# Optimization experiments

Hardware: AMD Instinct MI355X
Metric: run time of the kernel (lower is better)

## Reference

```python
import jax, jax.numpy as jnp
import numpy as np

N = 256   # units (waveguides)
L = 256   # num_layers (rectangular mesh: L == N)
B = 16384 # batch
TWO_PI = 2.0 * np.pi


def _perm_indices():
    # Rectangular-mesh column permutations: alternate +/-1 circular shifts so
    # successive columns couple (0,1),(2,3),... then (1,2),(3,4),...; final
    # permutation undoes the net shift (perm_layers has L+1 entries).
    ar = np.arange(N)
    shifts = [0] + [(1 if l % 2 == 1 else -1) for l in range(1, L)]
    perms = [(ar + s) % N for s in shifts]
    perms.append((ar - sum(shifts)) % N)
    return np.asarray(perms, dtype=np.int32)  # (L+1, N)


def setup_inputs() -> dict:
    key = jax.random.key(0)
    ks = jax.random.split(key, 5)
    x_re = jax.random.normal(ks[0], (B, N), jnp.float32)
    x_im = jax.random.normal(ks[1], (B, N), jnp.float32)
    theta = jax.random.uniform(ks[2], (L, N // 2), jnp.float32) * TWO_PI
    phi = jax.random.uniform(ks[3], (L, N // 2), jnp.float32) * TWO_PI
    gamma = jax.random.uniform(ks[4], (N,), jnp.float32) * TWO_PI
    perm_idx = jnp.asarray(_perm_indices())
    pp = np.arange(N).reshape(-1, 2)[:, ::-1].reshape(-1)  # [1,0,3,2,...]
    pairwise_perm_idx = jnp.asarray(pp, dtype=jnp.int32)
    return dict(x_re=x_re, x_im=x_im, theta=theta, phi=phi, gamma=gamma,
                perm_idx=perm_idx, pairwise_perm_idx=pairwise_perm_idx)


def _mesh_diag_offdiag(theta, phi):
    # Bloch basis, differential internal arrangement: +theta/2 on top port
    # (even waveguide), -theta/2 on bottom port (odd waveguide).
    t = theta.T  # (N/2, L)
    internal = jnp.stack([t * 0.5, -t * 0.5], axis=1).reshape(N, L)
    # single-mode external arrangement: phi on top port, 0 on bottom.
    external = jnp.stack([phi.T, jnp.zeros_like(phi.T)], axis=1).reshape(N, L)
    ipsl = jnp.exp(1j * internal)   # (N, L) complex64
    epsl = jnp.exp(1j * external)
    up = lambda a: jnp.roll(a, -1, axis=0)   # roll_tensor(x, up=True)
    dn = lambda a: jnp.roll(a, 1, axis=0)    # roll_tensor(x)
    e = jnp.float32(0.5)  # ideal 50:50 splitters -> all mzi_error_tensors = 0.5
    # hadamard = False branch of Mesh.mesh_layers
    s11 = e * ipsl - e * up(ipsl)
    s22 = dn(-e * ipsl + e * up(ipsl))
    s12 = 1j * dn(e * ipsl + e * up(ipsl))
    s21 = 1j * (e * ipsl + e * up(ipsl))
    diag = epsl * (s11 + s22) * 0.5
    off = dn(epsl) * (s21 + s12) * 0.5
    return diag.T, off.T  # (L, N)


def reference(x_re, x_im, theta, phi, gamma, perm_idx, pairwise_perm_idx):
    diag, off = _mesh_diag_offdiag(theta, phi)
    # include_diagonal_phases: input phase screen exp(i*gamma)
    x = (x_re + 1j * x_im) * jnp.exp(1j * gamma)[None, :]

    def step(x, lay):
        perm, d, o = lay
        x = jnp.take(x, perm, axis=-1)                              # PermutationLayer
        x = x * d + jnp.take(x * o, pairwise_perm_idx, axis=-1)     # MZI couple
        return x, None

    x, _ = jax.lax.scan(step, x, (perm_idx[:L], diag, off))
    x = jnp.take(x, perm_idx[L], axis=-1)  # right_perm of final layer
    return jnp.stack([jnp.real(x), jnp.imag(x)])  # (2, B, N) float32
```

## Files before the change

### kernel.cpp

```cpp
#include <hip/hip_runtime.h>
#include <math.h>

#define NN 256
#define LL 256
#define BB 16384

typedef __attribute__((ext_vector_type(8))) short short8;
typedef __attribute__((ext_vector_type(4))) float f32x4;


__global__ void coef_kernel(const float* __restrict__ theta,
                            const float* __restrict__ phi,
                            const float* __restrict__ gamma,
                            float4* __restrict__ coef) {
    int idx = blockIdx.x * blockDim.x + threadIdx.x;
    if (idx >= LL * NN) return;
    int l = idx >> 8, j = idx & 255;
    int u = l & 1;
    int n = (j - u) & 255;
    int m = n ^ 1;
    const float* th = theta + l * (NN / 2);
    const float* ph = phi + l * (NN / 2);

    auto ipsl = [&](int k, double& re, double& im) {
        k &= 255;
        double a = (double)th[k >> 1] * ((k & 1) ? -0.5 : 0.5);
        double s, c; sincos(a, &s, &c); re = c; im = s;
    };
    double s, c;
    double inr, ini, ipr, ipi, imr, imi;
    ipsl(n, inr, ini); ipsl(n + 1, ipr, ipi); ipsl(n - 1, imr, imi);
    double enr = 1.0, eni = 0.0;
    if (!(n & 1)) { sincos((double)ph[n >> 1], &s, &c); enr = c; eni = s; }
    double dr = 2.0 * inr - ipr - imr;
    double di = 2.0 * ini - ipi - imi;
    double Dre = 0.25 * (enr * dr - eni * di);
    double Dim = 0.25 * (enr * di + eni * dr);
    ipsl(m, inr, ini); ipsl(m + 1, ipr, ipi); ipsl(m - 1, imr, imi);
    int mm = (m - 1) & 255;
    double emr = 1.0, emi = 0.0;
    if (!(mm & 1)) { sincos((double)ph[mm >> 1], &s, &c); emr = c; emi = s; }
    double orv = 2.0 * inr + ipr + imr;
    double oiv = 2.0 * ini + ipi + imi;
    double tre = emr * orv - emi * oiv;
    double tim = emr * oiv + emi * orv;
    double Ore = -0.25 * tim;
    double Oim =  0.25 * tre;

    if (l == 0) {
        double gs, gc;
        sincos((double)gamma[j], &gs, &gc);
        double a2 = Dre * gc - Dim * gs, b2 = Dre * gs + Dim * gc;
        Dre = a2; Dim = b2;
        sincos((double)gamma[j ^ 1], &gs, &gc);
        a2 = Ore * gc - Oim * gs; b2 = Ore * gs + Oim * gc;
        Ore = a2; Oim = b2;
    }
    coef[l * 256 + (j & 7) * 32 + (j >> 3)] =
        make_float4((float)Dre, (float)Dim, (float)Ore, (float)Oim);
}

__device__ __forceinline__ float2 mzi(float2 cD, float2 cO, float2 y, float2 p) {
    float2 t;
    asm("v_pk_mul_f32 %0, %1, %2 op_sel:[1,1] op_sel_hi:[1,0] neg_lo:[1,0]"
        : "=v"(t) : "v"(cO), "v"(p));
    asm("v_pk_fma_f32 %0, %1, %2, %0 op_sel:[0,0,0] op_sel_hi:[0,1,1]"
        : "+v"(t) : "v"(cO), "v"(p));
    asm("v_pk_fma_f32 %0, %1, %2, %0 op_sel:[1,1,0] op_sel_hi:[1,0,1] neg_lo:[1,0,0]"
        : "+v"(t) : "v"(cD), "v"(y));
    asm("v_pk_fma_f32 %0, %1, %2, %0 op_sel:[0,0,0] op_sel_hi:[0,1,1]"
        : "+v"(t) : "v"(cD), "v"(y));
    return t;
}
__device__ __forceinline__ float2 D_(float4 c) { return make_float2(c.x, c.y); }
__device__ __forceinline__ float2 O_(float4 c) { return make_float2(c.z, c.w); }

__global__ __launch_bounds__(256) void prop_kernel(const float4* __restrict__ coef,
                                                   float2* __restrict__ PA,
                                                   float2* __restrict__ PB) {
    const int lane = threadIdx.x & 63;
    const int wave = threadIdx.x >> 6;
    const int l32  = lane & 31;
    const int half = lane >> 5;
    const int gid  = blockIdx.x * 4 + wave;
    const int mhalf = gid >> 7;
    const int row  = ((gid & 127) << 1) | half;
    const int l0   = mhalf ? 128 : 0;
    const int idxL4 = (((lane & 32) | ((lane - 1) & 31))) << 2;
    const int idxR4 = (((lane & 32) | ((lane + 1) & 31))) << 2;

    float2 y[8];
#pragma unroll
    for (int j = 0; j < 8; ++j)
        y[j] = make_float2((8 * l32 + j == row) ? 1.f : 0.f, 0.f);

    const float4* cp = coef + l32;
    auto loadl = [&](int l, float4& c0, float4& c1, float4& c2, float4& c3,
                            float4& c4, float4& c5, float4& c6, float4& c7) {
        const float4* p = cp + l * 256;
        c0 = p[0 * 32]; c1 = p[1 * 32]; c2 = p[2 * 32]; c3 = p[3 * 32];
        c4 = p[4 * 32]; c5 = p[5 * 32]; c6 = p[6 * 32]; c7 = p[7 * 32];
    };

    float4 a0, a1, a2, a3, a4, a5, a6, a7;
    float4 b0, b1, b2, b3, b4, b5, b6, b7;
    loadl(l0, a0, a1, a2, a3, a4, a5, a6, a7);

#pragma unroll 1
    for (int it = 0; it < 64; ++it) {
        loadl(l0 + 2 * it + 1, b0, b1, b2, b3, b4, b5, b6, b7);
        {
            float2 t0 = y[0], t1 = y[1], t2 = y[2], t3 = y[3];
            float2 t4 = y[4], t5 = y[5], t6 = y[6], t7 = y[7];
            y[0] = mzi(D_(a0), O_(a0), t0, t1);
            y[1] = mzi(D_(a1), O_(a1), t1, t0);
            y[2] = mzi(D_(a2), O_(a2), t2, t3);
            y[3] = mzi(D_(a3), O_(a3), t3, t2);
            y[4] = mzi(D_(a4), O_(a4), t4, t5);
            y[5] = mzi(D_(a5), O_(a5), t5, t4);
            y[6] = mzi(D_(a6), O_(a6), t6, t7);
            y[7] = mzi(D_(a7), O_(a7), t7, t6);
        }
        if (it < 63) loadl(l0 + 2 * it + 2, a0, a1, a2, a3, a4, a5, a6, a7);
        {
            float2 t0 = y[0], t1 = y[1], t2 = y[2], t3 = y[3];
            float2 t4 = y[4], t5 = y[5], t6 = y[6], t7 = y[7];
            float2 plo, phi2;
            plo.x  = __int_as_float(__builtin_amdgcn_ds_bpermute(idxL4, __float_as_int(t7.x)));
            plo.y  = __int_as_float(__builtin_amdgcn_ds_bpermute(idxL4, __float_as_int(t7.y)));
            phi2.x = __int_as_float(__builtin_amdgcn_ds_bpermute(idxR4, __float_as_int(t0.x)));
            phi2.y = __int_as_float(__builtin_amdgcn_ds_bpermute(idxR4, __float_as_int(t0.y)));
            y[1] = mzi(D_(b1), O_(b1), t1, t2);
            y[2] = mzi(D_(b2), O_(b2), t2, t1);
            y[3] = mzi(D_(b3), O_(b3), t3, t4);
            y[4] = mzi(D_(b4), O_(b4), t4, t3);
            y[5] = mzi(D_(b5), O_(b5), t5, t6);
            y[6] = mzi(D_(b6), O_(b6), t6, t5);
            y[0] = mzi(D_(b0), O_(b0), t0, plo);
            y[7] = mzi(D_(b7), O_(b7), t7, phi2);
        }
    }

    float2* P = mhalf ? PB : PA;
#pragma unroll
    for (int j = 0; j < 8; ++j)
        P[row * 256 + 8 * l32 + j] = y[j];
}

__global__ __launch_bounds__(256) void combine_kernel(const float2* __restrict__ PA,
                                                      const float2* __restrict__ PB,
                                                      float2* __restrict__ Cm) {
    int i = blockIdx.x, j = threadIdx.x;
    float accr = 0.f, acci = 0.f;
#pragma unroll 4
    for (int k = 0; k < 256; ++k) {
        float2 a = PA[i * 256 + k];
        float2 b = PB[k * 256 + j];
        accr += a.x * b.x - a.y * b.y;
        acci += a.x * b.y + a.y * b.x;
    }
    Cm[i * 256 + j] = make_float2(accr, acci);
}

__device__ __forceinline__ unsigned short bf16rne(float f) {
    unsigned int u = __float_as_uint(f);
    unsigned int r = (u + 0x7FFFu + ((u >> 16) & 1u)) >> 16;
    return (unsigned short)r;
}
__device__ __forceinline__ float bf16f(unsigned short h) {
    return __uint_as_float(((unsigned int)h) << 16);
}
__device__ __forceinline__ void split3(float v, unsigned short& h0,
                                       unsigned short& h1, unsigned short& h2) {
    h0 = bf16rne(v);        float r1 = v - bf16f(h0);
    h1 = bf16rne(r1);       float r2 = r1 - bf16f(h1);
    h2 = bf16rne(r2);
}

__global__ __launch_bounds__(256) void wsplit_kernel(const float2* __restrict__ Cm,
                                                     unsigned short* __restrict__ Wt) {
    int idx = blockIdx.x * 256 + threadIdx.x;
    int n = idx >> 9, k = idx & 511;
    float w;
    if (k < 256) {
        float2 c = Cm[k * 256 + (n & 255)];
        w = (n < 256) ? c.x : c.y;
    } else {
        float2 c = Cm[(k - 256) * 256 + (n & 255)];
        w = (n < 256) ? -c.y : c.x;
    }
    unsigned short h0, h1, h2;
    split3(w, h0, h1, h2);
    Wt[0 * 262144 + n * 512 + k] = h0;
    Wt[1 * 262144 + n * 512 + k] = h1;
    Wt[2 * 262144 + n * 512 + k] = h2;
}

__global__ __launch_bounds__(256, 2) void gemm_kernel(
        const float* __restrict__ x_re, const float* __restrict__ x_im,
        const unsigned short* __restrict__ Wt, float* __restrict__ out) {
    __shared__ unsigned short XL[3][128][40];
    __shared__ unsigned short WL[3][128][40];

    const int t    = threadIdx.x;
    const int lane = t & 63;
    const int wave = t >> 6;
    const int wm   = wave >> 1, wn = wave & 1;
    const int nt = blockIdx.x & 3, mt = blockIdx.x >> 2;
    const int m0 = mt * 128, n0 = nt * 128;
    const int lr = lane & 15, lg = lane >> 4;

    f32x4 acc[4][4];
#pragma unroll
    for (int a = 0; a < 4; ++a)
#pragma unroll
        for (int b = 0; b < 4; ++b) acc[a][b] = (f32x4)0.f;

#pragma unroll 1
    for (int ks = 0; ks < 16; ++ks) {
        const int k0 = ks * 32;
        const float* xsrc = (k0 < 256) ? x_re : x_im;
        const int kcol = k0 & 255;
#pragma unroll
        for (int r = 0; r < 4; ++r) {
            int F = r * 256 + t;
            int row = F >> 3, g = F & 7;
            float4 v = ((const float4*)xsrc)[(m0 + row) * 64 + (kcol >> 2) + g];
            unsigned short h0[4], h1[4], h2[4];
            split3(v.x, h0[0], h1[0], h2[0]);
            split3(v.y, h0[1], h1[1], h2[1]);
            split3(v.z, h0[2], h1[2], h2[2]);
            split3(v.w, h0[3], h1[3], h2[3]);
            *(ushort4*)&XL[0][row][g * 4] = make_ushort4(h0[0], h0[1], h0[2], h0[3]);
            *(ushort4*)&XL[1][row][g * 4] = make_ushort4(h1[0], h1[1], h1[2], h1[3]);
            *(ushort4*)&XL[2][row][g * 4] = make_ushort4(h2[0], h2[1], h2[2], h2[3]);
        }
#pragma unroll
        for (int r = 0; r < 6; ++r) {
            int U = r * 256 + t;
            int p = U >> 9, rem = U & 511;
            int n = rem >> 2, ku = (rem & 3) * 8;
            uint4 v = ((const uint4*)Wt)[p * 32768 + (n0 + n) * 64 + ((k0 + ku) >> 3)];
            *(uint4*)&WL[p][n][ku] = v;
        }
        __syncthreads();

        short8 bfr[3][4];
#pragma unroll
        for (int p = 0; p < 3; ++p)
#pragma unroll
            for (int ni = 0; ni < 4; ++ni)
                bfr[p][ni] = *(const short8*)&WL[p][wn * 64 + ni * 16 + lr][lg * 8];

#pragma unroll
        for (int i = 0; i < 3; ++i) {
            short8 af[4];
#pragma unroll
            for (int mi = 0; mi < 4; ++mi)
                af[mi] = *(const short8*)&XL[i][wm * 64 + mi * 16 + lr][lg * 8];
#pragma unroll
            for (int j = 0; j < 3; ++j) {
                if (i + j > 2) continue;
#pragma unroll
                for (int mi = 0; mi < 4; ++mi)
#pragma unroll
                    for (int ni = 0; ni < 4; ++ni)
                        acc[mi][ni] = __builtin_amdgcn_mfma_f32_16x16x32_bf16(
                            af[mi], bfr[j][ni], acc[mi][ni], 0, 0, 0);
            }
        }
        __syncthreads();
    }

#pragma unroll
    for (int mi = 0; mi < 4; ++mi) {
#pragma unroll
        for (int ni = 0; ni < 4; ++ni) {
            int nglob = n0 + wn * 64 + ni * 16 + lr;
            float* dst = (nglob < 256)
                       ? out + (size_t)(nglob)
                       : out + (size_t)BB * 256 + (nglob - 256);
#pragma unroll
            for (int e = 0; e < 4; ++e) {
                int m = m0 + wm * 64 + mi * 16 + lg * 4 + e;
                dst[(size_t)m * 256] = acc[mi][ni][e];
            }
        }
    }
}

extern "C" void kernel_launch(void* const* d_in, const int* in_sizes, int n_in,
                              void* d_out, int out_size, void* d_ws, size_t ws_size,
                              hipStream_t stream) {
    const float* x_re  = (const float*)d_in[0];
    const float* x_im  = (const float*)d_in[1];
    const float* theta = (const float*)d_in[2];
    const float* phi   = (const float*)d_in[3];
    const float* gamma = (const float*)d_in[4];

    char* ws = (char*)d_ws;
    float4* coef        = (float4*)ws;
    float2* PA          = (float2*)(ws + (1 << 20));
    float2* PB          = (float2*)(ws + (1 << 20) + (512 << 10));
    float2* Cm          = (float2*)(ws + (2 << 20));
    unsigned short* Wt  = (unsigned short*)(ws + (2 << 20) + (512 << 10));

    hipLaunchKernelGGL(coef_kernel, dim3(256), dim3(256), 0, stream,
                       theta, phi, gamma, coef);
    hipLaunchKernelGGL(prop_kernel, dim3(64), dim3(256), 0, stream, coef, PA, PB);
    hipLaunchKernelGGL(combine_kernel, dim3(256), dim3(256), 0, stream, PA, PB, Cm);
    hipLaunchKernelGGL(wsplit_kernel, dim3(1024), dim3(256), 0, stream, Cm, Wt);
    hipLaunchKernelGGL(gemm_kernel, dim3(512), dim3(256), 0, stream,
                       x_re, x_im, Wt, (float*)d_out);
}
```

Measured before the change: 198.1 us.

## Precompute sincos tables, fuse combine with weight split, prefetch GEMM tiles

After: 238.4 us. +20.4%, slower.

```diff
diff --git a/kernel.cpp b/kernel.cpp
--- a/kernel.cpp
+++ b/kernel.cpp
@@ -9,8 +9,21 @@
 typedef __attribute__((ext_vector_type(4))) float f32x4;
 
 
-__global__ void coef_kernel(const float* __restrict__ theta,
-                            const float* __restrict__ phi,
+__global__ void tab_kernel(const float* __restrict__ theta,
+                           const float* __restrict__ phi,
+                           double2* __restrict__ ipt,
+                           double2* __restrict__ ept) {
+    int idx = blockIdx.x * blockDim.x + threadIdx.x;
+    if (idx >= LL * 128) return;
+    double s, c;
+    sincos((double)theta[idx] * 0.5, &s, &c);
+    ipt[idx] = make_double2(c, s);
+    sincos((double)phi[idx], &s, &c);
+    ept[idx] = make_double2(c, s);
+}
+
+__global__ void coef_kernel(const double2* __restrict__ ipt,
+                            const double2* __restrict__ ept,
                             const float* __restrict__ gamma,
                             float4* __restrict__ coef) {
     int idx = blockIdx.x * blockDim.x + threadIdx.x;
@@ -19,19 +32,18 @@
     int u = l & 1;
     int n = (j - u) & 255;
     int m = n ^ 1;
-    const float* th = theta + l * (NN / 2);
-    const float* ph = phi + l * (NN / 2);
+    const double2* ip = ipt + l * 128;
+    const double2* ep = ept + l * 128;
 
     auto ipsl = [&](int k, double& re, double& im) {
         k &= 255;
-        double a = (double)th[k >> 1] * ((k & 1) ? -0.5 : 0.5);
-        double s, c; sincos(a, &s, &c); re = c; im = s;
+        double2 v = ip[k >> 1];
+        re = v.x; im = (k & 1) ? -v.y : v.y;
     };
-    double s, c;
     double inr, ini, ipr, ipi, imr, imi;
     ipsl(n, inr, ini); ipsl(n + 1, ipr, ipi); ipsl(n - 1, imr, imi);
     double enr = 1.0, eni = 0.0;
-    if (!(n & 1)) { sincos((double)ph[n >> 1], &s, &c); enr = c; eni = s; }
+    if (!(n & 1)) { double2 v = ep[n >> 1]; enr = v.x; eni = v.y; }
     double dr = 2.0 * inr - ipr - imr;
     double di = 2.0 * ini - ipi - imi;
     double Dre = 0.25 * (enr * dr - eni * di);
@@ -39,7 +51,7 @@
     ipsl(m, inr, ini); ipsl(m + 1, ipr, ipi); ipsl(m - 1, imr, imi);
     int mm = (m - 1) & 255;
     double emr = 1.0, emi = 0.0;
-    if (!(mm & 1)) { sincos((double)ph[mm >> 1], &s, &c); emr = c; emi = s; }
+    if (!(mm & 1)) { double2 v = ep[mm >> 1]; emr = v.x; emi = v.y; }
     double orv = 2.0 * inr + ipr + imr;
     double oiv = 2.0 * ini + ipi + imi;
     double tre = emr * orv - emi * oiv;
@@ -48,12 +60,12 @@
     double Oim =  0.25 * tre;
 
     if (l == 0) {
-        double gs, gc;
-        sincos((double)gamma[j], &gs, &gc);
-        double a2 = Dre * gc - Dim * gs, b2 = Dre * gs + Dim * gc;
+        double s, c;
+        sincos((double)gamma[j], &s, &c);
+        double a2 = Dre * c - Dim * s, b2 = Dre * s + Dim * c;
         Dre = a2; Dim = b2;
-        sincos((double)gamma[j ^ 1], &gs, &gc);
-        a2 = Ore * gc - Oim * gs; b2 = Ore * gs + Oim * gc;
+        sincos((double)gamma[j ^ 1], &s, &c);
+        a2 = Ore * c - Oim * s; b2 = Ore * s + Oim * c;
         Ore = a2; Oim = b2;
     }
     coef[l * 256 + (j & 7) * 32 + (j >> 3)] =
@@ -83,23 +95,27 @@
     const int l32  = lane & 31;
     const int half = lane >> 5;
     const int gid  = blockIdx.x * 4 + wave;
-    const int mhalf = gid >> 7;
-    const int row  = ((gid & 127) << 1) | half;
+    const int mhalf = gid >> 6;
+    const int c4   = (gid & 63) * 4;
     const int l0   = mhalf ? 128 : 0;
     const int idxL4 = (((lane & 32) | ((lane - 1) & 31))) << 2;
     const int idxR4 = (((lane & 32) | ((lane + 1) & 31))) << 2;
 
-    float2 y[8];
-#pragma unroll
-    for (int j = 0; j < 8; ++j)
-        y[j] = make_float2((8 * l32 + j == row) ? 1.f : 0.f, 0.f);
+    float2 y[2][8];
+#pragma unroll
+    for (int s2 = 0; s2 < 2; ++s2) {
+        int row = c4 + 2 * s2 + half;
+#pragma unroll
+        for (int j = 0; j < 8; ++j)
+            y[s2][j] = make_float2((8 * l32 + j == row) ? 1.f : 0.f, 0.f);
+    }
 
     const float4* cp = coef + l32;
     auto loadl = [&](int l, float4& c0, float4& c1, float4& c2, float4& c3,
-                            float4& c4, float4& c5, float4& c6, float4& c7) {
+                            float4& c4_, float4& c5, float4& c6, float4& c7) {
         const float4* p = cp + l * 256;
         c0 = p[0 * 32]; c1 = p[1 * 32]; c2 = p[2 * 32]; c3 = p[3 * 32];
-        c4 = p[4 * 32]; c5 = p[5 * 32]; c6 = p[6 * 32]; c7 = p[7 * 32];
+        c4_ = p[4 * 32]; c5 = p[5 * 32]; c6 = p[6 * 32]; c7 = p[7 * 32];
     };
 
     float4 a0, a1, a2, a3, a4, a5, a6, a7;
@@ -109,123 +125,136 @@
 #pragma unroll 1
     for (int it = 0; it < 64; ++it) {
         loadl(l0 + 2 * it + 1, b0, b1, b2, b3, b4, b5, b6, b7);
-        {
-            float2 t0 = y[0], t1 = y[1], t2 = y[2], t3 = y[3];
-            float2 t4 = y[4], t5 = y[5], t6 = y[6], t7 = y[7];
-            y[0] = mzi(D_(a0), O_(a0), t0, t1);
-            y[1] = mzi(D_(a1), O_(a1), t1, t0);
-            y[2] = mzi(D_(a2), O_(a2), t2, t3);
-            y[3] = mzi(D_(a3), O_(a3), t3, t2);
-            y[4] = mzi(D_(a4), O_(a4), t4, t5);
-            y[5] = mzi(D_(a5), O_(a5), t5, t4);
-            y[6] = mzi(D_(a6), O_(a6), t6, t7);
-            y[7] = mzi(D_(a7), O_(a7), t7, t6);
+#pragma unroll
+        for (int s2 = 0; s2 < 2; ++s2) {
+            float2 t0 = y[s2][0], t1 = y[s2][1], t2 = y[s2][2], t3 = y[s2][3];
+            float2 t4 = y[s2][4], t5 = y[s2][5], t6 = y[s2][6], t7 = y[s2][7];
+            y[s2][0] = mzi(D_(a0), O_(a0), t0, t1);
+            y[s2][1] = mzi(D_(a1), O_(a1), t1, t0);
+            y[s2][2] = mzi(D_(a2), O_(a2), t2, t3);
+            y[s2][3] = mzi(D_(a3), O_(a3), t3, t2);
+            y[s2][4] = mzi(D_(a4), O_(a4), t4, t5);
+            y[s2][5] = mzi(D_(a5), O_(a5), t5, t4);
+            y[s2][6] = mzi(D_(a6), O_(a6), t6, t7);
+            y[s2][7] = mzi(D_(a7), O_(a7), t7, t6);
         }
         if (it < 63) loadl(l0 + 2 * it + 2, a0, a1, a2, a3, a4, a5, a6, a7);
-        {
-            float2 t0 = y[0], t1 = y[1], t2 = y[2], t3 = y[3];
-            float2 t4 = y[4], t5 = y[5], t6 = y[6], t7 = y[7];
+#pragma unroll
+        for (int s2 = 0; s2 < 2; ++s2) {
+            float2 t0 = y[s2][0], t1 = y[s2][1], t2 = y[s2][2], t3 = y[s2][3];
+            float2 t4 = y[s2][4], t5 = y[s2][5], t6 = y[s2][6], t7 = y[s2][7];
             float2 plo, phi2;
             plo.x  = __int_as_float(__builtin_amdgcn_ds_bpermute(idxL4, __float_as_int(t7.x)));
             plo.y  = __int_as_float(__builtin_amdgcn_ds_bpermute(idxL4, __float_as_int(t7.y)));
             phi2.x = __int_as_float(__builtin_amdgcn_ds_bpermute(idxR4, __float_as_int(t0.x)));
             phi2.y = __int_as_float(__builtin_amdgcn_ds_bpermute(idxR4, __float_as_int(t0.y)));
-            y[1] = mzi(D_(b1), O_(b1), t1, t2);
-            y[2] = mzi(D_(b2), O_(b2), t2, t1);
-            y[3] = mzi(D_(b3), O_(b3), t3, t4);
-            y[4] = mzi(D_(b4), O_(b4), t4, t3);
-            y[5] = mzi(D_(b5), O_(b5), t5, t6);
-            y[6] = mzi(D_(b6), O_(b6), t6, t5);
-            y[0] = mzi(D_(b0), O_(b0), t0, plo);
-            y[7] = mzi(D_(b7), O_(b7), t7, phi2);
+            y[s2][1] = mzi(D_(b1), O_(b1), t1, t2);
+            y[s2][2] = mzi(D_(b2), O_(b2), t2, t1);
+            y[s2][3] = mzi(D_(b3), O_(b3), t3, t4);
+            y[s2][4] = mzi(D_(b4), O_(b4), t4, t3);
+            y[s2][5] = mzi(D_(b5), O_(b5), t5, t6);
+            y[s2][6] = mzi(D_(b6), O_(b6), t6, t5);
+            y[s2][0] = mzi(D_(b0), O_(b0), t0, plo);
+            y[s2][7] = mzi(D_(b7), O_(b7), t7, phi2);
         }
     }
 
     float2* P = mhalf ? PB : PA;
 #pragma unroll
-    for (int j = 0; j < 8; ++j)
-        P[row * 256 + 8 * l32 + j] = y[j];
-}
-
-__global__ __launch_bounds__(256) void combine_kernel(const float2* __restrict__ PA,
-                                                      const float2* __restrict__ PB,
-                                                      float2* __restrict__ Cm) {
+    for (int s2 = 0; s2 < 2; ++s2) {
+        int row = c4 + 2 * s2 + half;
+#pragma unroll
+        for (int j = 0; j < 8; ++j)
+            P[row * 256 + 8 * l32 + j] = y[s2][j];
+    }
+}
+
+__device__ __forceinline__ unsigned short bf16rne(float f) {
+    unsigned int u2 = __float_as_uint(f);
+    unsigned int r = (u2 + 0x7FFFu + ((u2 >> 16) & 1u)) >> 16;
+    return (unsigned short)r;
+}
+__device__ __forceinline__ float bf16f(unsigned short h) {
+    return __uint_as_float(((unsigned int)h) << 16);
+}
+__device__ __forceinline__ void split3(float v, unsigned short& h0,
+                                       unsigned short& h1, unsigned short& h2) {
+    h0 = bf16rne(v);        float r1 = v - bf16f(h0);
+    h1 = bf16rne(r1);       float r2 = r1 - bf16f(h1);
+    h2 = bf16rne(r2);
+}
+
+__global__ __launch_bounds__(256) void combineW_kernel(const float2* __restrict__ PA,
+                                                       const float2* __restrict__ PB,
+                                                       unsigned short* __restrict__ Wt) {
     int i = blockIdx.x, j = threadIdx.x;
     float accr = 0.f, acci = 0.f;
-#pragma unroll 4
+#pragma unroll 8
     for (int k = 0; k < 256; ++k) {
         float2 a = PA[i * 256 + k];
         float2 b = PB[k * 256 + j];
         accr += a.x * b.x - a.y * b.y;
         acci += a.x * b.y + a.y * b.x;
     }
-    Cm[i * 256 + j] = make_float2(accr, acci);
-}
-
-__device__ __forceinline__ unsigned short bf16rne(float f) {
-    unsigned int u = __float_as_uint(f);
-    unsigned int r = (u + 0x7FFFu + ((u >> 16) & 1u)) >> 16;
-    return (unsigned short)r;
-}
-__device__ __forceinline__ float bf16f(unsigned short h) {
-    return __uint_as_float(((unsigned int)h) << 16);
-}
-__device__ __forceinline__ void split3(float v, unsigned short& h0,
-                                       unsigned short& h1, unsigned short& h2) {
-    h0 = bf16rne(v);        float r1 = v - bf16f(h0);
-    h1 = bf16rne(r1);       float r2 = r1 - bf16f(h1);
-    h2 = bf16rne(r2);
-}
-
-__global__ __launch_bounds__(256) void wsplit_kernel(const float2* __restrict__ Cm,
-                                                     unsigned short* __restrict__ Wt) {
-    int idx = blockIdx.x * 256 + threadIdx.x;
-    int n = idx >> 9, k = idx & 511;
-    float w;
-    if (k < 256) {
-        float2 c = Cm[k * 256 + (n & 255)];
-        w = (n < 256) ? c.x : c.y;
-    } else {
-        float2 c = Cm[(k - 256) * 256 + (n & 255)];
-        w = (n < 256) ? -c.y : c.x;
-    }
-    unsigned short h0, h1, h2;
-    split3(w, h0, h1, h2);
-    Wt[0 * 262144 + n * 512 + k] = h0;
-    Wt[1 * 262144 + n * 512 + k] = h1;
-    Wt[2 * 262144 + n * 512 + k] = h2;
+    unsigned short r0, r1, r2, i0, i1, i2, n0, n1, n2;
+    split3(accr, r0, r1, r2);
+    split3(acci, i0, i1, i2);
+    split3(-acci, n0, n1, n2);
+    unsigned short* W0 = Wt;
+    unsigned short* W1 = Wt + 262144;
+    unsigned short* W2 = Wt + 524288;
+    W0[j * 512 + i] = r0;           W1[j * 512 + i] = r1;           W2[j * 512 + i] = r2;
+    W0[(j + 256) * 512 + i] = i0;   W1[(j + 256) * 512 + i] = i1;   W2[(j + 256) * 512 + i] = i2;
+    W0[j * 512 + i + 256] = n0;     W1[j * 512 + i + 256] = n1;     W2[j * 512 + i + 256] = n2;
+    W0[(j + 256) * 512 + i + 256] = r0;
+    W1[(j + 256) * 512 + i + 256] = r1;
+    W2[(j + 256) * 512 + i + 256] = r2;
 }
 
 __global__ __launch_bounds__(256, 2) void gemm_kernel(
         const float* __restrict__ x_re, const float* __restrict__ x_im,
         const unsigned short* __restrict__ Wt, float* __restrict__ out) {
-    __shared__ unsigned short XL[3][128][40];
-    __shared__ unsigned short WL[3][128][40];
+    __shared__ unsigned short XL[3][128][42];
+    __shared__ unsigned short WL[3][128][42];
 
     const int t    = threadIdx.x;
     const int lane = t & 63;
     const int wave = t >> 6;
     const int wm   = wave >> 1, wn = wave & 1;
-    const int nt = blockIdx.x & 3, mt = blockIdx.x >> 2;
+    const int Lb = (blockIdx.x & 7) * 64 + (blockIdx.x >> 3);
+    const int mt = Lb >> 2, nt = Lb & 3;
     const int m0 = mt * 128, n0 = nt * 128;
     const int lr = lane & 15, lg = lane >> 4;
 
-    f32x4 acc[4][4];
-#pragma unroll
-    for (int a = 0; a < 4; ++a)
-#pragma unroll
-        for (int b = 0; b < 4; ++b) acc[a][b] = (f32x4)0.f;
-
-#pragma unroll 1
-    for (int ks = 0; ks < 16; ++ks) {
+    float4 xv[4];
+    uint4  wv[6];
+    const int F   = t;
+    const int Un  = t;
+
+    auto load_tiles = [&](int ks) {
         const int k0 = ks * 32;
         const float* xsrc = (k0 < 256) ? x_re : x_im;
         const int kcol = k0 & 255;
 #pragma unroll
         for (int r = 0; r < 4; ++r) {
-            int F = r * 256 + t;
-            int row = F >> 3, g = F & 7;
-            float4 v = ((const float4*)xsrc)[(m0 + row) * 64 + (kcol >> 2) + g];
+            int Fi = r * 256 + F;
+            int row = Fi >> 3, g = Fi & 7;
+            xv[r] = ((const float4*)xsrc)[(m0 + row) * 64 + (kcol >> 2) + g];
+        }
+#pragma unroll
+        for (int r = 0; r < 6; ++r) {
+            int U = r * 256 + Un;
+            int p = U >> 9, rem = U & 511;
+            int n = rem >> 2, ku = (rem & 3) * 8;
+            wv[r] = ((const uint4*)Wt)[p * 32768 + (n0 + n) * 64 + ((k0 + ku) >> 3)];
+        }
+    };
+    auto write_tiles = [&]() {
+#pragma unroll
+        for (int r = 0; r < 4; ++r) {
+            int Fi = r * 256 + F;
+            int row = Fi >> 3, g = Fi & 7;
+            float4 v = xv[r];
             unsigned short h0[4], h1[4], h2[4];
             split3(v.x, h0[0], h1[0], h2[0]);
             split3(v.y, h0[1], h1[1], h2[1]);
@@ -237,13 +266,26 @@
         }
 #pragma unroll
         for (int r = 0; r < 6; ++r) {
-            int U = r * 256 + t;
+            int U = r * 256 + Un;
             int p = U >> 9, rem = U & 511;
             int n = rem >> 2, ku = (rem & 3) * 8;
-            uint4 v = ((const uint4*)Wt)[p * 32768 + (n0 + n) * 64 + ((k0 + ku) >> 3)];
-            *(uint4*)&WL[p][n][ku] = v;
-        }
-        __syncthreads();
+            *(uint4*)&WL[p][n][ku] = wv[r];
+        }
+    };
+
+    f32x4 acc[4][4];
+#pragma unroll
+    for (int a = 0; a < 4; ++a)
+#pragma unroll
+        for (int b = 0; b < 4; ++b) acc[a][b] = (f32x4)0.f;
+
+    load_tiles(0);
+    write_tiles();
+    __syncthreads();
+
+#pragma unroll 1
+    for (int ks = 0; ks < 16; ++ks) {
+        if (ks < 15) load_tiles(ks + 1);
 
         short8 bfr[3][4];
 #pragma unroll
@@ -251,7 +293,6 @@
 #pragma unroll
             for (int ni = 0; ni < 4; ++ni)
                 bfr[p][ni] = *(const short8*)&WL[p][wn * 64 + ni * 16 + lr][lg * 8];
-
 #pragma unroll
         for (int i = 0; i < 3; ++i) {
             short8 af[4];
@@ -259,16 +300,18 @@
             for (int mi = 0; mi < 4; ++mi)
                 af[mi] = *(const short8*)&XL[i][wm * 64 + mi * 16 + lr][lg * 8];
 #pragma unroll
-            for (int j = 0; j < 3; ++j) {
-                if (i + j > 2) continue;
+            for (int jj = 0; jj < 3; ++jj) {
+                if (i + jj > 2) continue;
 #pragma unroll
                 for (int mi = 0; mi < 4; ++mi)
 #pragma unroll
                     for (int ni = 0; ni < 4; ++ni)
                         acc[mi][ni] = __builtin_amdgcn_mfma_f32_16x16x32_bf16(
-                            af[mi], bfr[j][ni], acc[mi][ni], 0, 0, 0);
+                            af[mi], bfr[jj][ni], acc[mi][ni], 0, 0, 0);
             }
         }
+        __syncthreads();
+        if (ks < 15) write_tiles();
         __syncthreads();
     }
 
@@ -278,7 +321,7 @@
         for (int ni = 0; ni < 4; ++ni) {
             int nglob = n0 + wn * 64 + ni * 16 + lr;
             float* dst = (nglob < 256)
-                       ? out + (size_t)(nglob)
+                       ? out + (size_t)nglob
                        : out + (size_t)BB * 256 + (nglob - 256);
 #pragma unroll
             for (int e = 0; e < 4; ++e) {
@@ -302,14 +345,16 @@
     float4* coef        = (float4*)ws;
     float2* PA          = (float2*)(ws + (1 << 20));
     float2* PB          = (float2*)(ws + (1 << 20) + (512 << 10));
-    float2* Cm          = (float2*)(ws + (2 << 20));
-    unsigned short* Wt  = (unsigned short*)(ws + (2 << 20) + (512 << 10));
-
+    unsigned short* Wt  = (unsigned short*)(ws + (2 << 20));
+    double2* ipt        = (double2*)(ws + (3 << 20) + (512 << 10));
+    double2* ept        = (double2*)(ws + (4 << 20));
+
+    hipLaunchKernelGGL(tab_kernel, dim3(128), dim3(256), 0, stream,
+                       theta, phi, ipt, ept);
     hipLaunchKernelGGL(coef_kernel, dim3(256), dim3(256), 0, stream,
-                       theta, phi, gamma, coef);
-    hipLaunchKernelGGL(prop_kernel, dim3(64), dim3(256), 0, stream, coef, PA, PB);
-    hipLaunchKernelGGL(combine_kernel, dim3(256), dim3(256), 0, stream, PA, PB, Cm);
-    hipLaunchKernelGGL(wsplit_kernel, dim3(1024), dim3(256), 0, stream, Cm, Wt);
+                       ipt, ept, gamma, coef);
+    hipLaunchKernelGGL(prop_kernel, dim3(32), dim3(256), 0, stream, coef, PA, PB);
+    hipLaunchKernelGGL(combineW_kernel, dim3(256), dim3(256), 0, stream, PA, PB, Wt);
     hipLaunchKernelGGL(gemm_kernel, dim3(512), dim3(256), 0, stream,
                        x_re, x_im, Wt, (float*)d_out);
 }
```
